# Performance work log

Hardware: AMD Instinct MI355X
Metric: run time of the kernel (lower is better)

## Reference

```python
import jax, jax.numpy as jnp
import numpy as np

K = 1024
D = 512
DECAY = 0.99


def setup_inputs() -> dict:
    key = jax.random.key(0)
    k1, k2, k3 = jax.random.split(key, 3)
    z_e_x = jax.random.normal(k1, (64, 256, D), dtype=jnp.float32)
    codebook = jax.random.normal(k2, (K, D), dtype=jnp.float32)
    ema_count = jnp.ones((K,), dtype=jnp.float32)
    ema_w = jax.random.normal(k3, (K, D), dtype=jnp.float32)
    return {"z_e_x": z_e_x, "codebook": codebook,
            "ema_count": ema_count, "ema_w": ema_w}


def reference(z_e_x, codebook, ema_count, ema_w):
    # --- vector quantization: nearest codebook entry (squared L2) ---
    flat = z_e_x.reshape(-1, D)                       # [N, D]
    cb_sqr = jnp.sum(codebook ** 2, axis=1)           # [K]
    in_sqr = jnp.sum(flat ** 2, axis=1, keepdims=True)  # [N, 1]
    distances = (cb_sqr[None, :] + in_sqr) - 2.0 * (flat @ codebook.T)  # [N, K]
    indices = jnp.argmin(distances, axis=1)           # [N] int

    # straight-through codes from current codebook
    z_q_x = codebook[indices].reshape(z_e_x.shape)

    # --- EMA codebook update (training branch) ---
    counts = jnp.zeros((K,), dtype=flat.dtype).at[indices].add(1.0)       # sum of one-hots
    new_ema_count = DECAY * ema_count + (1.0 - DECAY) * counts
    dw = jnp.zeros((K, D), dtype=flat.dtype).at[indices].add(flat)        # one_hot.T @ flat
    new_ema_w = DECAY * ema_w + (1.0 - DECAY) * dw
    new_embedding = new_ema_w / new_ema_count[:, None]

    # codes from the updated codebook
    z_q_x_bar = new_embedding[indices].reshape(z_e_x.shape)

    return (z_q_x, z_q_x_bar, new_embedding, new_ema_count, new_ema_w)
```

## Files before the change

kernel.cpp:

```cpp
#include <hip/hip_runtime.h>

typedef _Float16 half8  __attribute__((ext_vector_type(8)));
typedef float    f32x4  __attribute__((ext_vector_type(4)));

constexpr int K_CODES = 1024;
constexpr int D_DIM   = 512;
constexpr float DECAY = 0.99f;
constexpr float OMD   = 0.01f;
constexpr float LO_SCALE = 2048.0f;
constexpr float INV_LO   = 1.0f / 2048.0f;

constexpr int BM = 128;
constexpr int BN = 128;
constexpr int BK = 32;
constexpr int TILE = BM * BK;
constexpr int NPART = K_CODES / BN;
constexpr int CHUNK = 32;

__global__ __launch_bounds__(256)
void prepsplit_kernel(const float* __restrict__ A, const float* __restrict__ cb,
                      float* __restrict__ cbsqr, float* __restrict__ counts,
                      _Float16* __restrict__ ah, _Float16* __restrict__ al,
                      _Float16* __restrict__ bh, _Float16* __restrict__ bl,
                      int nA) {
    int b = blockIdx.x;
    if (b < nA) {
        size_t i8 = ((size_t)b * 256 + threadIdx.x) * 8;
        f32x4 v0 = *reinterpret_cast<const f32x4*>(&A[i8]);
        f32x4 v1 = *reinterpret_cast<const f32x4*>(&A[i8 + 4]);
        half8 h, l;
        #pragma unroll
        for (int j = 0; j < 4; ++j) {
            _Float16 hh = (_Float16)v0[j];
            h[j] = hh;
            l[j] = (_Float16)((v0[j] - (float)hh) * LO_SCALE);
        }
        #pragma unroll
        for (int j = 0; j < 4; ++j) {
            _Float16 hh = (_Float16)v1[j];
            h[4 + j] = hh;
            l[4 + j] = (_Float16)((v1[j] - (float)hh) * LO_SCALE);
        }
        *reinterpret_cast<half8*>(&ah[i8]) = h;
        *reinterpret_cast<half8*>(&al[i8]) = l;
    } else {
        int w    = threadIdx.x >> 6;
        int lane = threadIdx.x & 63;
        int k = (b - nA) * 4 + w;
        size_t base = (size_t)k * D_DIM + lane * 8;
        f32x4 v0 = *reinterpret_cast<const f32x4*>(&cb[base]);
        f32x4 v1 = *reinterpret_cast<const f32x4*>(&cb[base + 4]);
        half8 h, l;
        float s = 0.f;
        #pragma unroll
        for (int j = 0; j < 4; ++j) {
            s += v0[j] * v0[j];
            _Float16 hh = (_Float16)v0[j];
            h[j] = hh;
            l[j] = (_Float16)((v0[j] - (float)hh) * LO_SCALE);
        }
        #pragma unroll
        for (int j = 0; j < 4; ++j) {
            s += v1[j] * v1[j];
            _Float16 hh = (_Float16)v1[j];
            h[4 + j] = hh;
            l[4 + j] = (_Float16)((v1[j] - (float)hh) * LO_SCALE);
        }
        *reinterpret_cast<half8*>(&bh[base]) = h;
        *reinterpret_cast<half8*>(&bl[base]) = l;
        #pragma unroll
        for (int off = 32; off > 0; off >>= 1) s += __shfl_down(s, off);
        if (lane == 0) { cbsqr[k] = s; counts[k] = 0.f; }
    }
}

__global__ __launch_bounds__(256, 2)
void argmin_mfma(const _Float16* __restrict__ Ah,
                 const _Float16* __restrict__ Al,
                 const _Float16* __restrict__ Bh,
                 const _Float16* __restrict__ Bl,
                 const float* __restrict__ cbsqr,
                 float* __restrict__ pval,
                 int*   __restrict__ pidx) {
    __shared__ _Float16 Ahs[2][TILE];
    __shared__ _Float16 Als[2][TILE];
    __shared__ _Float16 Bhs[2][TILE];
    __shared__ _Float16 Bls[2][TILE];
    __shared__ float    sv[2][BM];
    __shared__ int      si[2][BM];

    const int tid  = threadIdx.x;
    const int lane = tid & 63;
    const int wid  = tid >> 6;
    const int wr = wid >> 1, wc = wid & 1;
    const int lq = lane >> 4;
    const int lr = lane & 15;

    const int row0  = blockIdx.x * BM;
    const int cbase = blockIdx.y * BN;

    f32x4 acc_h[4][4], acc_c[4][4];
    #pragma unroll
    for (int m = 0; m < 4; ++m)
        #pragma unroll
        for (int n = 0; n < 4; ++n) {
            acc_h[m][n] = f32x4{0.f, 0.f, 0.f, 0.f};
            acc_c[m][n] = f32x4{0.f, 0.f, 0.f, 0.f};
        }

    auto stage = [&](int buf, int d0) {
        #pragma unroll
        for (int it = 0; it < 2; ++it) {
            int p = it * 4096 + wid * 1024 + lane * 16;
            int row  = p >> 6;
            int cpos = (p >> 4) & 3;
            int sc   = cpos ^ ((row ^ (row >> 2)) & 3);
            size_t aoff = (size_t)(row0 + row) * D_DIM + d0 + sc * 8;
            size_t boff = (size_t)(cbase + row) * D_DIM + d0 + sc * 8;
            int dst = it * 2048 + wid * 512;
            __builtin_amdgcn_global_load_lds(
                (const __attribute__((address_space(1))) void*)(Ah + aoff),
                (__attribute__((address_space(3))) void*)(&Ahs[buf][dst]), 16, 0, 0);
            __builtin_amdgcn_global_load_lds(
                (const __attribute__((address_space(1))) void*)(Al + aoff),
                (__attribute__((address_space(3))) void*)(&Als[buf][dst]), 16, 0, 0);
            __builtin_amdgcn_global_load_lds(
                (const __attribute__((address_space(1))) void*)(Bh + boff),
                (__attribute__((address_space(3))) void*)(&Bhs[buf][dst]), 16, 0, 0);
            __builtin_amdgcn_global_load_lds(
                (const __attribute__((address_space(1))) void*)(Bl + boff),
                (__attribute__((address_space(3))) void*)(&Bls[buf][dst]), 16, 0, 0);
        }
    };

    stage(0, 0);
    __syncthreads();

    constexpr int NSTEP = D_DIM / BK;
    for (int t = 0; t < NSTEP; ++t) {
        const int buf = t & 1;
        if (t + 1 < NSTEP) stage(buf ^ 1, (t + 1) * BK);

        half8 bh[4], bl[4];
        #pragma unroll
        for (int n = 0; n < 4; ++n) {
            int rB  = wc * 64 + n * 16 + lr;
            int pos = lq ^ ((rB ^ (rB >> 2)) & 3);
            bh[n] = *reinterpret_cast<const half8*>(&Bhs[buf][rB * 32 + pos * 8]);
            bl[n] = *reinterpret_cast<const half8*>(&Bls[buf][rB * 32 + pos * 8]);
        }
        #pragma unroll
        for (int m = 0; m < 4; ++m) {
            int rA  = wr * 64 + m * 16 + lr;
            int pos = lq ^ ((rA ^ (rA >> 2)) & 3);
            half8 ah = *reinterpret_cast<const half8*>(&Ahs[buf][rA * 32 + pos * 8]);
            half8 al = *reinterpret_cast<const half8*>(&Als[buf][rA * 32 + pos * 8]);
            #pragma unroll
            for (int n = 0; n < 4; ++n) {
                acc_h[m][n] = __builtin_amdgcn_mfma_f32_16x16x32_f16(ah, bh[n], acc_h[m][n], 0, 0, 0);
                acc_c[m][n] = __builtin_amdgcn_mfma_f32_16x16x32_f16(ah, bl[n], acc_c[m][n], 0, 0, 0);
                acc_c[m][n] = __builtin_amdgcn_mfma_f32_16x16x32_f16(al, bh[n], acc_c[m][n], 0, 0, 0);
            }
        }
        __syncthreads();
    }

    float cs[4];
    #pragma unroll
    for (int n = 0; n < 4; ++n) cs[n] = cbsqr[cbase + wc * 64 + n * 16 + lr];

    #pragma unroll
    for (int m = 0; m < 4; ++m) {
        #pragma unroll
        for (int q = 0; q < 4; ++q) {
            float bv = 3.4e38f;
            int   bi = 0;
            #pragma unroll
            for (int n = 0; n < 4; ++n) {
                float d = cs[n] - 2.0f * acc_h[m][n][q] - (2.0f * INV_LO) * acc_c[m][n][q];
                int   c = cbase + wc * 64 + n * 16 + lr;
                if (d < bv) { bv = d; bi = c; }
            }
            #pragma unroll
            for (int off = 1; off < 16; off <<= 1) {
                float v2 = __shfl_xor(bv, off);
                int   i2 = __shfl_xor(bi, off);
                if (v2 < bv || (v2 == bv && i2 < bi)) { bv = v2; bi = i2; }
            }
            if (lr == 0) {
                int prow = wr * 64 + m * 16 + lq * 4 + q;
                sv[wc][prow] = bv;
                si[wc][prow] = bi;
            }
        }
    }
    __syncthreads();
    if (tid < BM) {
        float v0 = sv[0][tid], v1 = sv[1][tid];
        int   i0 = si[0][tid], i1 = si[1][tid];
        float bv = (v1 < v0) ? v1 : v0;
        int   bi = (v1 < v0) ? i1 : i0;
        pval[(size_t)(row0 + tid) * NPART + blockIdx.y] = bv;
        pidx[(size_t)(row0 + tid) * NPART + blockIdx.y] = bi;
    }
}

__global__ __launch_bounds__(256)
void combine_kernel(const float* __restrict__ pval, const int* __restrict__ pidx,
                    int* __restrict__ indices, float* __restrict__ counts, int N) {
    int r = blockIdx.x * 256 + threadIdx.x;
    if (r >= N) return;
    float bv = pval[(size_t)r * NPART];
    int   bi = pidx[(size_t)r * NPART];
    #pragma unroll
    for (int p = 1; p < NPART; ++p) {
        float v = pval[(size_t)r * NPART + p];
        int  ii = pidx[(size_t)r * NPART + p];
        if (v < bv) { bv = v; bi = ii; }
    }
    indices[r] = bi;
    atomicAdd(&counts[bi], 1.0f);
}

__global__ __launch_bounds__(256)
void scan_kernel(const float* __restrict__ counts,
                 int* __restrict__ offs, int* __restrict__ cursor) {
    __shared__ int part[256];
    int t = threadIdx.x;
    int c[4], s = 0;
    #pragma unroll
    for (int j = 0; j < 4; ++j) { c[j] = (int)counts[t * 4 + j]; s += c[j]; }
    part[t] = s;
    __syncthreads();
    for (int off = 1; off < 256; off <<= 1) {
        int v   = part[t];
        int add = (t >= off) ? part[t - off] : 0;
        __syncthreads();
        part[t] = v + add;
        __syncthreads();
    }
    int run = part[t] - s;
    #pragma unroll
    for (int j = 0; j < 4; ++j) {
        offs[t * 4 + j]   = run;
        cursor[t * 4 + j] = run;
        run += c[j];
    }
    if (t == 255) offs[K_CODES] = part[255];
}

__global__ __launch_bounds__(256)
void zeroscatter_kernel(const int* __restrict__ indices, int* __restrict__ cursor,
                        int* __restrict__ packed, float4* __restrict__ dw,
                        int N, int nzero) {
    int b = blockIdx.x;
    if (b < nzero) {
        dw[b * 256 + threadIdx.x] = make_float4(0.f, 0.f, 0.f, 0.f);
    } else {
        int r = (b - nzero) * 256 + threadIdx.x;
        if (r >= N) return;
        int k = indices[r];
        int pos = atomicAdd(&cursor[k], 1);
        packed[pos] = (k << 16) | r;
    }
}

__global__ __launch_bounds__(128)
void chunksum_kernel(const float* __restrict__ flat, const int* __restrict__ packed,
                     float* __restrict__ dw, int N) {
    __shared__ int ent[CHUNK + 1];
    const int t = threadIdx.x;
    const int base = blockIdx.x * CHUNK;
    const int cnt = min(CHUNK, N - base);
    if (t < cnt) ent[t] = packed[base + t];
    if (t == cnt) ent[t] = -1;
    __syncthreads();

    f32x4 acc = {0.f, 0.f, 0.f, 0.f};
    for (int i0 = 0; i0 < cnt; i0 += 8) {
        const int m = min(8, cnt - i0);
        f32x4 v[8];
        #pragma unroll
        for (int j = 0; j < 8; ++j) {
            if (j < m) {
                int r = ent[i0 + j] & 0xFFFF;
                v[j] = *reinterpret_cast<const f32x4*>(&flat[(size_t)r * D_DIM + t * 4]);
            }
        }
        #pragma unroll
        for (int j = 0; j < 8; ++j) {
            if (j < m) {
                acc[0] += v[j][0]; acc[1] += v[j][1];
                acc[2] += v[j][2]; acc[3] += v[j][3];
                int k = ent[i0 + j] >> 16;
                if ((ent[i0 + j + 1] >> 16) != k) {
                    float* p = &dw[(size_t)k * D_DIM + t * 4];
                    atomicAdd(p + 0, acc[0]);
                    atomicAdd(p + 1, acc[1]);
                    atomicAdd(p + 2, acc[2]);
                    atomicAdd(p + 3, acc[3]);
                    acc = f32x4{0.f, 0.f, 0.f, 0.f};
                }
            }
        }
    }
}

__global__ __launch_bounds__(256)
void finalize_kernel(const float* __restrict__ ema_count, const float* __restrict__ ema_w,
                     const float* __restrict__ counts, const float* __restrict__ dw,
                     float* __restrict__ new_emb, float* __restrict__ new_count,
                     float* __restrict__ new_ema_w) {
    int gid = blockIdx.x * 256 + threadIdx.x;
    int k = gid >> 7;
    int d = (gid & 127) * 4;
    float nc = DECAY * ema_count[k] + OMD * counts[k];
    size_t off = (size_t)k * D_DIM + d;
    float4 w  = *reinterpret_cast<const float4*>(&ema_w[off]);
    float4 dv = *reinterpret_cast<const float4*>(&dw[off]);
    float4 nw;
    nw.x = DECAY * w.x + OMD * dv.x;
    nw.y = DECAY * w.y + OMD * dv.y;
    nw.z = DECAY * w.z + OMD * dv.z;
    nw.w = DECAY * w.w + OMD * dv.w;
    *reinterpret_cast<float4*>(&new_ema_w[off]) = nw;
    float inv = 1.0f / nc;
    float4 ne;
    ne.x = nw.x * inv; ne.y = nw.y * inv; ne.z = nw.z * inv; ne.w = nw.w * inv;
    *reinterpret_cast<float4*>(&new_emb[off]) = ne;
    if ((gid & 127) == 0) new_count[k] = nc;
}

__global__ __launch_bounds__(256)
void gather_kernel(const float* __restrict__ codebook, const float* __restrict__ new_emb,
                   const int* __restrict__ indices,
                   float* __restrict__ zq, float* __restrict__ zqb) {
    int gid = blockIdx.x * 256 + threadIdx.x;
    int r = gid >> 7;
    int d = (gid & 127) * 4;
    int k = indices[r];
    size_t src = (size_t)k * D_DIM + d;
    size_t dst = (size_t)r * D_DIM + d;
    *reinterpret_cast<float4*>(&zq[dst])  = *reinterpret_cast<const float4*>(&codebook[src]);
    *reinterpret_cast<float4*>(&zqb[dst]) = *reinterpret_cast<const float4*>(&new_emb[src]);
}

extern "C" void kernel_launch(void* const* d_in, const int* in_sizes, int n_in,
                              void* d_out, int out_size, void* d_ws, size_t ws_size,
                              hipStream_t stream) {
    const float* z_e_x     = (const float*)d_in[0];
    const float* codebook  = (const float*)d_in[1];
    const float* ema_count = (const float*)d_in[2];
    const float* ema_w     = (const float*)d_in[3];

    const int N = in_sizes[0] / D_DIM;

    float* out = (float*)d_out;
    float* z_q_x     = out;
    float* z_q_x_bar = z_q_x + (size_t)N * D_DIM;
    float* new_emb   = z_q_x_bar + (size_t)N * D_DIM;
    float* new_count = new_emb + (size_t)K_CODES * D_DIM;
    float* new_ema_w = new_count + K_CODES;

    _Float16* Ahp = (_Float16*)z_q_x_bar;
    _Float16* Alp = Ahp + (size_t)N * D_DIM;

    char* ws = (char*)d_ws;
    int*   indices = (int*)ws;
    float* cbsqr   = (float*)(ws + (size_t)N * 4);
    float* pval    = cbsqr + K_CODES;
    int*   pidx    = (int*)(pval + (size_t)N * NPART);
    float* counts  = (float*)(pidx + (size_t)N * NPART);
    _Float16* bh   = (_Float16*)(counts + K_CODES);
    _Float16* bl   = bh + (size_t)K_CODES * D_DIM;
    float* dw      = (float*)bh;
    int*   offs    = (int*)(bl + (size_t)K_CODES * D_DIM);
    int*   cursor  = offs + K_CODES + 1;
    int*   packed  = cursor + K_CODES;

    const int nA = (N * D_DIM / 8) / 256;
    prepsplit_kernel<<<nA + K_CODES / 4, 256, 0, stream>>>(
        z_e_x, codebook, cbsqr, counts, Ahp, Alp, bh, bl, nA);

    dim3 g_argmin(N / BM, K_CODES / BN);
    argmin_mfma<<<g_argmin, 256, 0, stream>>>(Ahp, Alp, bh, bl, cbsqr, pval, pidx);

    combine_kernel<<<(N + 255) / 256, 256, 0, stream>>>(pval, pidx, indices, counts, N);

    scan_kernel<<<1, 256, 0, stream>>>(counts, offs, cursor);

    const int nzero = (K_CODES * D_DIM / 4) / 256;
    zeroscatter_kernel<<<nzero + (N + 255) / 256, 256, 0, stream>>>(
        indices, cursor, packed, (float4*)dw, N, nzero);

    chunksum_kernel<<<(N + CHUNK - 1) / CHUNK, 128, 0, stream>>>(z_e_x, packed, dw, N);

    finalize_kernel<<<(K_CODES * (D_DIM / 4)) / 256, 256, 0, stream>>>(
        ema_count, ema_w, counts, dw, new_emb, new_count, new_ema_w);

    gather_kernel<<<(N * (D_DIM / 4)) / 256, 256, 0, stream>>>(
        codebook, new_emb, indices, z_q_x, z_q_x_bar);
}
```

Before: 140.7 us.

## Load A fragments directly from global in argmin GEMM and fuse finalize with gather

Result: slower. 168.5 us (+19.8%).

```diff
diff --git a/kernel.cpp b/kernel.cpp
--- a/kernel.cpp
+++ b/kernel.cpp
@@ -13,7 +13,7 @@
 constexpr int BM = 128;
 constexpr int BN = 128;
 constexpr int BK = 32;
-constexpr int TILE = BM * BK;
+constexpr int TILE = BN * BK;
 constexpr int NPART = K_CODES / BN;
 constexpr int CHUNK = 32;
 
@@ -82,10 +82,8 @@
                  const float* __restrict__ cbsqr,
                  float* __restrict__ pval,
                  int*   __restrict__ pidx) {
-    __shared__ _Float16 Ahs[2][TILE];
-    __shared__ _Float16 Als[2][TILE];
-    __shared__ _Float16 Bhs[2][TILE];
-    __shared__ _Float16 Bls[2][TILE];
+    __shared__ _Float16 Bhs[TILE];
+    __shared__ _Float16 Bls[TILE];
     __shared__ float    sv[2][BM];
     __shared__ int      si[2][BM];
 
@@ -99,6 +97,8 @@
     const int row0  = blockIdx.x * BM;
     const int cbase = blockIdx.y * BN;
 
+    const size_t aoff0 = (size_t)(row0 + wr * 64 + lr) * D_DIM + lq * 8;
+
     f32x4 acc_h[4][4], acc_c[4][4];
     #pragma unroll
     for (int m = 0; m < 4; ++m)
@@ -108,58 +108,51 @@
             acc_c[m][n] = f32x4{0.f, 0.f, 0.f, 0.f};
         }
 
-    auto stage = [&](int buf, int d0) {
+    constexpr int NSTEP = D_DIM / BK;
+    for (int t = 0; t < NSTEP; ++t) {
+        const int d0 = t * BK;
         #pragma unroll
         for (int it = 0; it < 2; ++it) {
             int p = it * 4096 + wid * 1024 + lane * 16;
             int row  = p >> 6;
             int cpos = (p >> 4) & 3;
             int sc   = cpos ^ ((row ^ (row >> 2)) & 3);
-            size_t aoff = (size_t)(row0 + row) * D_DIM + d0 + sc * 8;
             size_t boff = (size_t)(cbase + row) * D_DIM + d0 + sc * 8;
             int dst = it * 2048 + wid * 512;
             __builtin_amdgcn_global_load_lds(
-                (const __attribute__((address_space(1))) void*)(Ah + aoff),
-                (__attribute__((address_space(3))) void*)(&Ahs[buf][dst]), 16, 0, 0);
-            __builtin_amdgcn_global_load_lds(
-                (const __attribute__((address_space(1))) void*)(Al + aoff),
-                (__attribute__((address_space(3))) void*)(&Als[buf][dst]), 16, 0, 0);
-            __builtin_amdgcn_global_load_lds(
                 (const __attribute__((address_space(1))) void*)(Bh + boff),
-                (__attribute__((address_space(3))) void*)(&Bhs[buf][dst]), 16, 0, 0);
+                (__attribute__((address_space(3))) void*)(Bhs + dst), 16, 0, 0);
             __builtin_amdgcn_global_load_lds(
                 (const __attribute__((address_space(1))) void*)(Bl + boff),
-                (__attribute__((address_space(3))) void*)(&Bls[buf][dst]), 16, 0, 0);
-        }
-    };
-
-    stage(0, 0);
-    __syncthreads();
-
-    constexpr int NSTEP = D_DIM / BK;
-    for (int t = 0; t < NSTEP; ++t) {
-        const int buf = t & 1;
-        if (t + 1 < NSTEP) stage(buf ^ 1, (t + 1) * BK);
+                (__attribute__((address_space(3))) void*)(Bls + dst), 16, 0, 0);
+        }
+        half8 ah[4], al[4];
+        ah[0] = *reinterpret_cast<const half8*>(Ah + aoff0 + 0 * 16 * D_DIM + d0);
+        al[0] = *reinterpret_cast<const half8*>(Al + aoff0 + 0 * 16 * D_DIM + d0);
+        ah[1] = *reinterpret_cast<const half8*>(Ah + aoff0 + 1 * 16 * D_DIM + d0);
+        al[1] = *reinterpret_cast<const half8*>(Al + aoff0 + 1 * 16 * D_DIM + d0);
+        __syncthreads();
 
         half8 bh[4], bl[4];
         #pragma unroll
         for (int n = 0; n < 4; ++n) {
             int rB  = wc * 64 + n * 16 + lr;
             int pos = lq ^ ((rB ^ (rB >> 2)) & 3);
-            bh[n] = *reinterpret_cast<const half8*>(&Bhs[buf][rB * 32 + pos * 8]);
-            bl[n] = *reinterpret_cast<const half8*>(&Bls[buf][rB * 32 + pos * 8]);
-        }
+            bh[n] = *reinterpret_cast<const half8*>(&Bhs[rB * 32 + pos * 8]);
+            bl[n] = *reinterpret_cast<const half8*>(&Bls[rB * 32 + pos * 8]);
+        }
+        ah[2] = *reinterpret_cast<const half8*>(Ah + aoff0 + 2 * 16 * D_DIM + d0);
+        al[2] = *reinterpret_cast<const half8*>(Al + aoff0 + 2 * 16 * D_DIM + d0);
+        ah[3] = *reinterpret_cast<const half8*>(Ah + aoff0 + 3 * 16 * D_DIM + d0);
+        al[3] = *reinterpret_cast<const half8*>(Al + aoff0 + 3 * 16 * D_DIM + d0);
+
         #pragma unroll
         for (int m = 0; m < 4; ++m) {
-            int rA  = wr * 64 + m * 16 + lr;
-            int pos = lq ^ ((rA ^ (rA >> 2)) & 3);
-            half8 ah = *reinterpret_cast<const half8*>(&Ahs[buf][rA * 32 + pos * 8]);
-            half8 al = *reinterpret_cast<const half8*>(&Als[buf][rA * 32 + pos * 8]);
             #pragma unroll
             for (int n = 0; n < 4; ++n) {
-                acc_h[m][n] = __builtin_amdgcn_mfma_f32_16x16x32_f16(ah, bh[n], acc_h[m][n], 0, 0, 0);
-                acc_c[m][n] = __builtin_amdgcn_mfma_f32_16x16x32_f16(ah, bl[n], acc_c[m][n], 0, 0, 0);
-                acc_c[m][n] = __builtin_amdgcn_mfma_f32_16x16x32_f16(al, bh[n], acc_c[m][n], 0, 0, 0);
+                acc_h[m][n] = __builtin_amdgcn_mfma_f32_16x16x32_f16(ah[m], bh[n], acc_h[m][n], 0, 0, 0);
+                acc_c[m][n] = __builtin_amdgcn_mfma_f32_16x16x32_f16(ah[m], bl[n], acc_c[m][n], 0, 0, 0);
+                acc_c[m][n] = __builtin_amdgcn_mfma_f32_16x16x32_f16(al[m], bh[n], acc_c[m][n], 0, 0, 0);
             }
         }
         __syncthreads();
@@ -307,42 +300,49 @@
 }
 
 __global__ __launch_bounds__(256)
-void finalize_kernel(const float* __restrict__ ema_count, const float* __restrict__ ema_w,
-                     const float* __restrict__ counts, const float* __restrict__ dw,
-                     float* __restrict__ new_emb, float* __restrict__ new_count,
-                     float* __restrict__ new_ema_w) {
-    int gid = blockIdx.x * 256 + threadIdx.x;
-    int k = gid >> 7;
-    int d = (gid & 127) * 4;
-    float nc = DECAY * ema_count[k] + OMD * counts[k];
-    size_t off = (size_t)k * D_DIM + d;
-    float4 w  = *reinterpret_cast<const float4*>(&ema_w[off]);
-    float4 dv = *reinterpret_cast<const float4*>(&dw[off]);
-    float4 nw;
-    nw.x = DECAY * w.x + OMD * dv.x;
-    nw.y = DECAY * w.y + OMD * dv.y;
-    nw.z = DECAY * w.z + OMD * dv.z;
-    nw.w = DECAY * w.w + OMD * dv.w;
-    *reinterpret_cast<float4*>(&new_ema_w[off]) = nw;
-    float inv = 1.0f / nc;
-    float4 ne;
-    ne.x = nw.x * inv; ne.y = nw.y * inv; ne.z = nw.z * inv; ne.w = nw.w * inv;
-    *reinterpret_cast<float4*>(&new_emb[off]) = ne;
-    if ((gid & 127) == 0) new_count[k] = nc;
-}
-
-__global__ __launch_bounds__(256)
-void gather_kernel(const float* __restrict__ codebook, const float* __restrict__ new_emb,
-                   const int* __restrict__ indices,
-                   float* __restrict__ zq, float* __restrict__ zqb) {
-    int gid = blockIdx.x * 256 + threadIdx.x;
-    int r = gid >> 7;
-    int d = (gid & 127) * 4;
-    int k = indices[r];
-    size_t src = (size_t)k * D_DIM + d;
-    size_t dst = (size_t)r * D_DIM + d;
-    *reinterpret_cast<float4*>(&zq[dst])  = *reinterpret_cast<const float4*>(&codebook[src]);
-    *reinterpret_cast<float4*>(&zqb[dst]) = *reinterpret_cast<const float4*>(&new_emb[src]);
+void tail_kernel(const float* __restrict__ codebook,
+                 const float* __restrict__ ema_count, const float* __restrict__ ema_w,
+                 const float* __restrict__ counts, const float* __restrict__ dw,
+                 const int* __restrict__ indices,
+                 float* __restrict__ new_emb, float* __restrict__ new_count,
+                 float* __restrict__ new_ema_w,
+                 float* __restrict__ zq, float* __restrict__ zqb, int nfin) {
+    int b = blockIdx.x;
+    if (b < nfin) {
+        int gid = b * 256 + threadIdx.x;
+        int k = gid >> 7;
+        int d = (gid & 127) * 4;
+        float nc = DECAY * ema_count[k] + OMD * counts[k];
+        size_t off = (size_t)k * D_DIM + d;
+        f32x4 w  = *reinterpret_cast<const f32x4*>(&ema_w[off]);
+        f32x4 dv = *reinterpret_cast<const f32x4*>(&dw[off]);
+        f32x4 nw, ne;
+        float inv = 1.0f / nc;
+        #pragma unroll
+        for (int j = 0; j < 4; ++j) {
+            nw[j] = DECAY * w[j] + OMD * dv[j];
+            ne[j] = nw[j] * inv;
+        }
+        *reinterpret_cast<f32x4*>(&new_ema_w[off]) = nw;
+        *reinterpret_cast<f32x4*>(&new_emb[off])   = ne;
+        if ((gid & 127) == 0) new_count[k] = nc;
+    } else {
+        int gid = (b - nfin) * 256 + threadIdx.x;
+        int r = gid >> 7;
+        int d = (gid & 127) * 4;
+        int k = indices[r];
+        size_t src = (size_t)k * D_DIM + d;
+        size_t dst = (size_t)r * D_DIM + d;
+        float nc = DECAY * ema_count[k] + OMD * counts[k];
+        float inv = 1.0f / nc;
+        f32x4 w  = *reinterpret_cast<const f32x4*>(&ema_w[src]);
+        f32x4 dv = *reinterpret_cast<const f32x4*>(&dw[src]);
+        f32x4 zb;
+        #pragma unroll
+        for (int j = 0; j < 4; ++j) zb[j] = (DECAY * w[j] + OMD * dv[j]) * inv;
+        *reinterpret_cast<f32x4*>(&zqb[dst]) = zb;
+        *reinterpret_cast<f32x4*>(&zq[dst])  = *reinterpret_cast<const f32x4*>(&codebook[src]);
+    }
 }
 
 extern "C" void kernel_launch(void* const* d_in, const int* in_sizes, int n_in,
@@ -395,9 +395,8 @@
 
     chunksum_kernel<<<(N + CHUNK - 1) / CHUNK, 128, 0, stream>>>(z_e_x, packed, dw, N);
 
-    finalize_kernel<<<(K_CODES * (D_DIM / 4)) / 256, 256, 0, stream>>>(
-        ema_count, ema_w, counts, dw, new_emb, new_count, new_ema_w);
-
-    gather_kernel<<<(N * (D_DIM / 4)) / 256, 256, 0, stream>>>(
-        codebook, new_emb, indices, z_q_x, z_q_x_bar);
-}
+    const int nfin = (K_CODES * D_DIM / 4) / 256;
+    tail_kernel<<<nfin + (N * D_DIM / 4) / 256, 256, 0, stream>>>(
+        codebook, ema_count, ema_w, counts, dw, indices,
+        new_emb, new_count, new_ema_w, z_q_x, z_q_x_bar, nfin);
+}
```
